# Kernel optimization log

Hardware: AMD Instinct MI355X
Metric: run time of the kernel (lower is better)

Reference implementation:

```python
import jax, jax.numpy as jnp
import numpy as np

N_PAPER = 50000
N_AUTHOR = 50000
E = 400000
N_FEAT = 256
N_HID = 256
N_CLASS = 128
TEMP = 1.0  # cfg.temparature


def setup_inputs() -> dict:
    key = jax.random.key(0)
    ks = jax.random.split(key, 40)
    def lin_init(k, shape, fan_in):
        s = 1.0 / np.sqrt(fan_in)
        return jax.random.uniform(k, shape, jnp.float32, -s, s)
    inp = {}
    inp['x_paper'] = jax.random.normal(ks[0], (N_PAPER, N_FEAT), jnp.float32)
    # xavier-uniform embedding for featureless node type 'author'
    xs = np.sqrt(6.0 / (N_AUTHOR + N_FEAT))
    inp['emb_author'] = jax.random.uniform(ks[1], (N_AUTHOR, N_FEAT), jnp.float32, -xs, xs)
    i = 2
    for l, fin in [(0, N_FEAT), (1, N_HID)]:
        for nt in ['paper', 'author']:
            inp[f'l{l}_root_{nt}_W'] = lin_init(ks[i], (fin, N_HID), fin); i += 1
            inp[f'l{l}_root_{nt}_b'] = lin_init(ks[i], (N_HID,), fin); i += 1
        for et in ['writes', 'rev', 'cites']:
            inp[f'l{l}_rel_{et}_W'] = lin_init(ks[i], (fin, N_HID), fin); i += 1
    inp['out_W'] = lin_init(ks[i], (N_HID, N_CLASS), N_HID); i += 1
    inp['out_b'] = lin_init(ks[i], (N_CLASS,), N_HID); i += 1
    inp['writes_src'] = jax.random.randint(ks[i], (E,), 0, N_AUTHOR); i += 1
    inp['writes_dst'] = jax.random.randint(ks[i], (E,), 0, N_PAPER); i += 1
    inp['rev_src'] = jax.random.randint(ks[i], (E,), 0, N_PAPER); i += 1
    inp['rev_dst'] = jax.random.randint(ks[i], (E,), 0, N_AUTHOR); i += 1
    inp['cites_src'] = jax.random.randint(ks[i], (E,), 0, N_PAPER); i += 1
    inp['cites_dst'] = jax.random.randint(ks[i], (E,), 0, N_PAPER); i += 1
    return inp


def _mean_agg(x_src, src, dst, n_dst):
    # sparse adj_t.matmul(x, reduce='mean'): segment-sum of gathered rows / in-degree (0 for isolated)
    msg = jax.ops.segment_sum(x_src[src], dst, num_segments=n_dst)  # [n_dst, d]
    deg = jax.ops.segment_sum(jnp.ones(src.shape[0], x_src.dtype), dst, num_segments=n_dst)
    return jnp.where(deg[:, None] > 0, msg / jnp.maximum(deg, 1.0)[:, None], 0.0)


def reference(x_paper, emb_author,
              l0_root_paper_W, l0_root_paper_b, l0_root_author_W, l0_root_author_b,
              l0_rel_writes_W, l0_rel_rev_W, l0_rel_cites_W,
              l1_root_paper_W, l1_root_paper_b, l1_root_author_W, l1_root_author_b,
              l1_rel_writes_W, l1_rel_rev_W, l1_rel_cites_W,
              out_W, out_b,
              writes_src, writes_dst, rev_src, rev_dst, cites_src, cites_dst):
    nnodes = {'paper': x_paper.shape[0], 'author': emb_author.shape[0]}
    # (src_type, dst_type, src_idx, dst_idx, rel_slot)
    edges = [('author', 'paper', writes_src, writes_dst, 0),
             ('paper', 'author', rev_src, rev_dst, 1),
             ('paper', 'paper', cites_src, cites_dst, 2)]
    layers = [
        {'root': {'paper': (l0_root_paper_W, l0_root_paper_b), 'author': (l0_root_author_W, l0_root_author_b)},
         'rel': [l0_rel_writes_W, l0_rel_rev_W, l0_rel_cites_W]},
        {'root': {'paper': (l1_root_paper_W, l1_root_paper_b), 'author': (l1_root_author_W, l1_root_author_b)},
         'rel': [l1_rel_writes_W, l1_rel_rev_W, l1_rel_cites_W]},
    ]
    xd = {'paper': x_paper, 'author': emb_author}
    xd_ = dict(xd)  # twin path starts from same features
    hs, hs_ = [], []
    for p in layers:
        out = {k: xd[k] @ p['root'][k][0] + p['root'][k][1] for k in xd}
        out_ = {k: xd_[k] @ p['root'][k][0] + p['root'][k][1] for k in xd_}
        for s, d, src, dst, slot in edges:
            W = p['rel'][slot]
            out[d] = out[d] + _mean_agg(xd[s], src, dst, nnodes[d]) @ W
            out_[d] = out_[d] + xd_[d] @ W  # twin path: no propagation, same rel transform
        xd = {k: jax.nn.relu(v) for k, v in out.items()}   # dropout is identity (eval)
        xd_ = {k: jax.nn.relu(v) for k, v in out_.items()}
        hs.append(xd['paper'])
        hs_.append(xd_['paper'])
    # Summarize: per-node dot-product attention over layer representations
    H = jnp.stack(hs)    # [L, N, d]
    H_ = jnp.stack(hs_)  # [L, N, d]
    alpha = jax.nn.softmax(jnp.sum(H * H_, axis=-1) / TEMP, axis=0)  # [L, N]
    h = jnp.sum(alpha[..., None] * H, axis=0)  # [N, d]
    logits = h @ out_W + out_b
    return (logits, alpha)
```

## Files before the change

kernel.cpp:

```cpp
#include <hip/hip_runtime.h>
#include <hip/hip_bf16.h>

#define NFEAT 256
#define BM 64
#define BN 64
#define BK 16

typedef __attribute__((ext_vector_type(8))) short bf16x8;
typedef __attribute__((ext_vector_type(4))) float f32x4;
typedef __attribute__((ext_vector_type(8))) unsigned short us8;

__device__ __forceinline__ void f2hilo(float x, unsigned short& h, unsigned short& l) {
    __hip_bfloat16 hb = __float2bfloat16(x);
    float hf = __bfloat162float(hb);
    __hip_bfloat16 lb = __float2bfloat16(x - hf);
    h = *reinterpret_cast<unsigned short*>(&hb);
    l = *reinterpret_cast<unsigned short*>(&lb);
}

__global__ __launch_bounds__(256) void addw3_kernel(const float* __restrict__ a,
                                                    const float* __restrict__ b,
                                                    const float* __restrict__ c,
                                                    float* __restrict__ o, int n) {
    int i = blockIdx.x * 256 + threadIdx.x;
    if (i < n) o[i] = a[i] + b[i] + c[i];
}

__global__ __launch_bounds__(256) void cvtW_kernel(const float* __restrict__ W, int K, int N,
                                                   unsigned short* __restrict__ Th,
                                                   unsigned short* __restrict__ Tl) {
    int idx = blockIdx.x * 256 + threadIdx.x;
    if (idx >= K * N) return;
    int k = idx / N, c = idx - k * N;
    unsigned short h, l;
    f2hilo(W[idx], h, l);
    Th[(size_t)c * K + k] = h;
    Tl[(size_t)c * K + k] = l;
}

__global__ __launch_bounds__(256) void deg_int_kernel(const int* __restrict__ dst,
                                                      int* __restrict__ deg, int nE) {
    int e = blockIdx.x * 256 + threadIdx.x;
    if (e < nE) atomicAdd(&deg[dst[e]], 1);
}

__global__ __launch_bounds__(256) void scan_p1(const int* __restrict__ deg, int n,
                                               int* __restrict__ off, int* __restrict__ bsum) {
    __shared__ int tmp[256];
    int tid = threadIdx.x;
    int i = blockIdx.x * 256 + tid;
    tmp[tid] = (i < n) ? deg[i] : 0;
    __syncthreads();
    #pragma unroll
    for (int ofs = 1; ofs < 256; ofs <<= 1) {
        int t = (tid >= ofs) ? tmp[tid - ofs] : 0;
        __syncthreads();
        tmp[tid] += t;
        __syncthreads();
    }
    if (i < n) off[i + 1] = tmp[tid];
    if (tid == 255) bsum[blockIdx.x] = tmp[255];
}

__global__ __launch_bounds__(256) void scan_p2(int* __restrict__ bA, int nA,
                                               int* __restrict__ bB, int nB,
                                               int* __restrict__ bC, int nC) {
    int* bs; int nb;
    if (blockIdx.x == 0) { bs = bA; nb = nA; }
    else if (blockIdx.x == 1) { bs = bB; nb = nB; }
    else { bs = bC; nb = nC; }
    __shared__ int tmp[256];
    int tid = threadIdx.x;
    tmp[tid] = (tid < nb) ? bs[tid] : 0;
    __syncthreads();
    #pragma unroll
    for (int ofs = 1; ofs < 256; ofs <<= 1) {
        int t = (tid >= ofs) ? tmp[tid - ofs] : 0;
        __syncthreads();
        tmp[tid] += t;
        __syncthreads();
    }
    if (tid < nb) bs[tid] = tmp[tid];
}

__global__ __launch_bounds__(256) void scan_p3(int n, int* __restrict__ off,
                                               const int* __restrict__ bsum) {
    int i = blockIdx.x * 256 + threadIdx.x;
    if (i == 0) off[0] = 0;
    if (i >= n) return;
    int b = blockIdx.x;
    if (b > 0) off[i + 1] += bsum[b - 1];
}

__global__ __launch_bounds__(256) void fill_csr_kernel(const int* __restrict__ src,
                                                       const int* __restrict__ dst, int nE,
                                                       const int* __restrict__ off,
                                                       int* __restrict__ cursor,
                                                       int* __restrict__ list) {
    int e = blockIdx.x * 256 + threadIdx.x;
    if (e >= nE) return;
    int d = dst[e];
    int pos = atomicAdd(&cursor[d], 1);
    list[off[d] + pos] = src[e];
}

__global__ __launch_bounds__(256) void agg_csr_kernel(const float* __restrict__ T,
                                                      const int* __restrict__ off,
                                                      const int* __restrict__ list,
                                                      float* __restrict__ D,
                                                      int do_relu, int M) {
    int r = blockIdx.x * 4 + (threadIdx.x >> 6);
    if (r >= M) return;
    int lane = threadIdx.x & 63;
    int start = off[r], end = off[r + 1];
    float4 acc = make_float4(0.f, 0.f, 0.f, 0.f);
    for (int e = start; e < end; ++e) {
        int s = list[e];
        float4 v = ((const float4*)(T + (size_t)s * NFEAT))[lane];
        acc.x += v.x; acc.y += v.y; acc.z += v.z; acc.w += v.w;
    }
    int cnt = end - start;
    float inv = (cnt > 0) ? 1.0f / (float)cnt : 0.0f;
    float4 d = ((float4*)(D + (size_t)r * NFEAT))[lane];
    d.x += acc.x * inv; d.y += acc.y * inv;
    d.z += acc.z * inv; d.w += acc.w * inv;
    if (do_relu) {
        d.x = fmaxf(d.x, 0.f); d.y = fmaxf(d.y, 0.f);
        d.z = fmaxf(d.z, 0.f); d.w = fmaxf(d.w, 0.f);
    }
    ((float4*)(D + (size_t)r * NFEAT))[lane] = d;
}

__global__ __launch_bounds__(256) void rowdot_kernel(const float* __restrict__ A,
                                                     const float* __restrict__ B,
                                                     float* __restrict__ s, int M) {
    int n = blockIdx.x * 4 + (threadIdx.x >> 6);
    if (n >= M) return;
    int lane = threadIdx.x & 63;
    float4 a = ((const float4*)(A + (size_t)n * NFEAT))[lane];
    float4 b = ((const float4*)(B + (size_t)n * NFEAT))[lane];
    float d = a.x * b.x + a.y * b.y + a.z * b.z + a.w * b.w;
    #pragma unroll
    for (int off = 32; off > 0; off >>= 1) d += __shfl_down(d, off);
    if (lane == 0) s[n] = d;
}

__global__ __launch_bounds__(256) void combine_kernel(const float* __restrict__ P1,
                                                      const float* __restrict__ P2,
                                                      const float* __restrict__ s0,
                                                      const float* __restrict__ s1,
                                                      float* __restrict__ h,
                                                      float* __restrict__ alpha,
                                                      int M) {
    int n = blockIdx.x * 4 + (threadIdx.x >> 6);
    if (n >= M) return;
    int lane = threadIdx.x & 63;
    float v0 = s0[n], v1 = s1[n];
    float m = fmaxf(v0, v1);
    float e0 = expf(v0 - m), e1 = expf(v1 - m);
    float inv = 1.0f / (e0 + e1);
    float a0 = e0 * inv, a1 = e1 * inv;
    float4 p1 = ((const float4*)(P1 + (size_t)n * NFEAT))[lane];
    float4 p2 = ((const float4*)(P2 + (size_t)n * NFEAT))[lane];
    float4 hv;
    hv.x = a0 * p1.x + a1 * p2.x;
    hv.y = a0 * p1.y + a1 * p2.y;
    hv.z = a0 * p1.z + a1 * p2.z;
    hv.w = a0 * p1.w + a1 * p2.w;
    ((float4*)(h + (size_t)n * NFEAT))[lane] = hv;
    if (lane == 0) {
        alpha[n]     = a0;
        alpha[M + n] = a1;
    }
}

__global__ __launch_bounds__(256, 2) void gemm_mfma(
    const float* __restrict__ X,
    const unsigned short* __restrict__ Wh,
    const unsigned short* __restrict__ Wl,
    const float* __restrict__ bias, int do_relu,
    float* __restrict__ C, int M, int N)
{
    __shared__ unsigned short Ah[128][40];
    __shared__ unsigned short Al[128][40];
    __shared__ unsigned short Bh[128][40];
    __shared__ unsigned short Bl[128][40];

    int tid = threadIdx.x;
    int lane = tid & 63;
    int w = tid >> 6;
    int wr = w >> 1, wc = w & 1;
    int row0 = blockIdx.x * 128, col0 = blockIdx.y * 128;

    int sr = tid >> 1;
    int sk = (tid & 1) * 16;

    int grow = row0 + sr; if (grow >= M) grow = M - 1;
    const float* Xrow = X + (size_t)grow * NFEAT;
    const unsigned short* Whrow = Wh + (size_t)(col0 + sr) * NFEAT;
    const unsigned short* Wlrow = Wl + (size_t)(col0 + sr) * NFEAT;

    f32x4 acc[4][4];
    #pragma unroll
    for (int m = 0; m < 4; ++m)
        #pragma unroll
        for (int n = 0; n < 4; ++n)
            acc[m][n] = (f32x4)(0.f);

    int fr = lane & 15;
    int fg = lane >> 4;

    for (int k0 = 0; k0 < NFEAT; k0 += 32) {
        unsigned short hh[16], ll[16];
        #pragma unroll
        for (int q = 0; q < 4; ++q) {
            float4 v = *(const float4*)(Xrow + k0 + sk + q * 4);
            f2hilo(v.x, hh[q*4+0], ll[q*4+0]);
            f2hilo(v.y, hh[q*4+1], ll[q*4+1]);
            f2hilo(v.z, hh[q*4+2], ll[q*4+2]);
            f2hilo(v.w, hh[q*4+3], ll[q*4+3]);
        }
        us8 bh0 = *(const us8*)(Whrow + k0 + sk);
        us8 bh1 = *(const us8*)(Whrow + k0 + sk + 8);
        us8 bl0 = *(const us8*)(Wlrow + k0 + sk);
        us8 bl1 = *(const us8*)(Wlrow + k0 + sk + 8);
        __syncthreads();
        *(us8*)&Ah[sr][sk]     = *(us8*)&hh[0];
        *(us8*)&Ah[sr][sk + 8] = *(us8*)&hh[8];
        *(us8*)&Al[sr][sk]     = *(us8*)&ll[0];
        *(us8*)&Al[sr][sk + 8] = *(us8*)&ll[8];
        *(us8*)&Bh[sr][sk]     = bh0;
        *(us8*)&Bh[sr][sk + 8] = bh1;
        *(us8*)&Bl[sr][sk]     = bl0;
        *(us8*)&Bl[sr][sk + 8] = bl1;
        __syncthreads();

        bf16x8 ah[4], al[4], bhf[4], blf[4];
        #pragma unroll
        for (int m = 0; m < 4; ++m) {
            int r = wr * 64 + m * 16 + fr;
            ah[m] = *(const bf16x8*)&Ah[r][fg * 8];
            al[m] = *(const bf16x8*)&Al[r][fg * 8];
        }
        #pragma unroll
        for (int n = 0; n < 4; ++n) {
            int c = wc * 64 + n * 16 + fr;
            bhf[n] = *(const bf16x8*)&Bh[c][fg * 8];
            blf[n] = *(const bf16x8*)&Bl[c][fg * 8];
        }
        #pragma unroll
        for (int m = 0; m < 4; ++m)
            #pragma unroll
            for (int n = 0; n < 4; ++n) {
                acc[m][n] = __builtin_amdgcn_mfma_f32_16x16x32_bf16(ah[m], bhf[n], acc[m][n], 0, 0, 0);
                acc[m][n] = __builtin_amdgcn_mfma_f32_16x16x32_bf16(al[m], bhf[n], acc[m][n], 0, 0, 0);
                acc[m][n] = __builtin_amdgcn_mfma_f32_16x16x32_bf16(ah[m], blf[n], acc[m][n], 0, 0, 0);
            }
    }

    #pragma unroll
    for (int n = 0; n < 4; ++n) {
        int c = col0 + wc * 64 + n * 16 + fr;
        float bv = bias ? bias[c] : 0.f;
        #pragma unroll
        for (int m = 0; m < 4; ++m) {
            int rbase = row0 + wr * 64 + m * 16 + fg * 4;
            #pragma unroll
            for (int i = 0; i < 4; ++i) {
                int r = rbase + i;
                if (r < M) {
                    float v = acc[m][n][i] + bv;
                    if (do_relu) v = fmaxf(v, 0.f);
                    C[(size_t)r * N + c] = v;
                }
            }
        }
    }
}

__global__ __launch_bounds__(256) void gemm_rowdot_kernel(
    const float* __restrict__ X, const float* __restrict__ W,
    const float* __restrict__ bias, const float* __restrict__ P,
    float* __restrict__ s, int M)
{
    __shared__ float Xs[BK][BM];
    __shared__ float Ws[BK][BN];
    __shared__ float srow[BM];

    int tid = threadIdx.x;
    int row0 = blockIdx.x * BM;

    int lr = tid & 63;
    int lk = (tid >> 6) * 4;
    int wk = tid >> 4;
    int wc = (tid & 15) * 4;
    int ty = tid >> 4;
    int tx = tid & 15;

    int grow = row0 + lr;
    if (grow >= M) grow = M - 1;

    if (tid < BM) srow[tid] = 0.f;

    float rp[4] = {0.f, 0.f, 0.f, 0.f};

    for (int col0 = 0; col0 < NFEAT; col0 += BN) {
        float acc[4][4] = {{0.f}};
        for (int k0 = 0; k0 < NFEAT; k0 += BK) {
            float4 xv = *(const float4*)(X + (size_t)grow * NFEAT + k0 + lk);
            float4 wv = *(const float4*)(W + (size_t)(k0 + wk) * NFEAT + col0 + wc);
            __syncthreads();
            Xs[lk + 0][lr] = xv.x;
            Xs[lk + 1][lr] = xv.y;
            Xs[lk + 2][lr] = xv.z;
            Xs[lk + 3][lr] = xv.w;
            *(float4*)&Ws[wk][wc] = wv;
            __syncthreads();
            #pragma unroll
            for (int kk = 0; kk < BK; ++kk) {
                float4 a = *(const float4*)&Xs[kk][ty * 4];
                float4 b = *(const float4*)&Ws[kk][tx * 4];
                acc[0][0] += a.x * b.x; acc[0][1] += a.x * b.y;
                acc[0][2] += a.x * b.z; acc[0][3] += a.x * b.w;
                acc[1][0] += a.y * b.x; acc[1][1] += a.y * b.y;
                acc[1][2] += a.y * b.z; acc[1][3] += a.y * b.w;
                acc[2][0] += a.z * b.x; acc[2][1] += a.z * b.y;
                acc[2][2] += a.z * b.z; acc[2][3] += a.z * b.w;
                acc[3][0] += a.w * b.x; acc[3][1] += a.w * b.y;
                acc[3][2] += a.w * b.z; acc[3][3] += a.w * b.w;
            }
        }
        int c0 = col0 + tx * 4;
        #pragma unroll
        for (int i = 0; i < 4; ++i) {
            int r = row0 + ty * 4 + i;
            if (r >= M) continue;
            float4 p = *(const float4*)(P + (size_t)r * NFEAT + c0);
            float v0 = fmaxf(acc[i][0] + bias[c0 + 0], 0.f);
            float v1 = fmaxf(acc[i][1] + bias[c0 + 1], 0.f);
            float v2 = fmaxf(acc[i][2] + bias[c0 + 2], 0.f);
            float v3 = fmaxf(acc[i][3] + bias[c0 + 3], 0.f);
            rp[i] += v0 * p.x + v1 * p.y + v2 * p.z + v3 * p.w;
        }
    }
    __syncthreads();
    #pragma unroll
    for (int i = 0; i < 4; ++i) atomicAdd(&srow[ty * 4 + i], rp[i]);
    __syncthreads();
    if (tid < BM && row0 + tid < M) s[row0 + tid] = srow[tid];
}

extern "C" void kernel_launch(void* const* d_in, const int* in_sizes, int n_in,
                              void* d_out, int out_size, void* d_ws, size_t ws_size,
                              hipStream_t stream)
{
    const float* x_paper    = (const float*)d_in[0];
    const float* emb_author = (const float*)d_in[1];
    const float* W0rp = (const float*)d_in[2];
    const float* b0rp = (const float*)d_in[3];
    const float* W0ra = (const float*)d_in[4];
    const float* b0ra = (const float*)d_in[5];
    const float* W0w  = (const float*)d_in[6];
    const float* W0rev= (const float*)d_in[7];
    const float* W0c  = (const float*)d_in[8];
    const float* W1rp = (const float*)d_in[9];
    const float* b1rp = (const float*)d_in[10];
    const float* W1w  = (const float*)d_in[13];
    const float* W1c  = (const float*)d_in[15];
    const float* outW = (const float*)d_in[16];
    const float* outb = (const float*)d_in[17];
    const int* w_src = (const int*)d_in[18];
    const int* w_dst = (const int*)d_in[19];
    const int* r_src = (const int*)d_in[20];
    const int* r_dst = (const int*)d_in[21];
    const int* c_src = (const int*)d_in[22];
    const int* c_dst = (const int*)d_in[23];

    const int NP = in_sizes[0] / NFEAT;
    const int NA = in_sizes[1] / NFEAT;
    const int NC = in_sizes[17];
    const int nEw = in_sizes[18], nEr = in_sizes[20], nEc = in_sizes[22];

    size_t NB = (size_t)(NP > NA ? NP : NA) * NFEAT;
    float* Z1 = (float*)d_ws;
    float* Z2 = Z1 + NB;
    float* Z3 = Z2 + NB;
    float* s0   = Z3 + NB;
    float* s1   = s0 + NP;
    float* Wc0f = s1 + NP;
    float* Wc1f = Wc0f + NFEAT * NFEAT;
    unsigned short* Wt = (unsigned short*)(Wc1f + NFEAT * NFEAT);
    const size_t WSLOT = 2 * 65536;
    #define WT_HI(i) (Wt + (size_t)(i) * WSLOT)
    #define WT_LO(i) (Wt + (size_t)(i) * WSLOT + 65536)
    int* ib   = (int*)(Wt + 11 * WSLOT);
    int* degW = ib;
    int* degR = degW + NP;
    int* degC = degR + NA;
    int* curW = degC + NP;
    int* curR = curW + NP;
    int* curC = curR + NA;
    int* offW = curC + NP;
    int* offR = offW + NP + 1;
    int* offC = offR + NA + 1;
    int* bsW  = offC + NP + 1;
    int* bsR  = bsW + 256;
    int* bsC  = bsR + 256;
    int* listW = bsC + 256;
    int* listR = listW + nEw;
    int* listC = listR + nEr;

    float* out   = (float*)d_out;
    float* alpha = out + (size_t)NP * NC;

    hipMemsetAsync(degW, 0, (size_t)2 * (NP + NA + NP) * sizeof(int), stream);

    deg_int_kernel<<<(nEw + 255) / 256, 256, 0, stream>>>(w_dst, degW, nEw);
    deg_int_kernel<<<(nEr + 255) / 256, 256, 0, stream>>>(r_dst, degR, nEr);
    deg_int_kernel<<<(nEc + 255) / 256, 256, 0, stream>>>(c_dst, degC, nEc);

    int nbP = (NP + 255) / 256, nbA = (NA + 255) / 256;
    scan_p1<<<nbP, 256, 0, stream>>>(degW, NP, offW, bsW);
    scan_p1<<<nbA, 256, 0, stream>>>(degR, NA, offR, bsR);
    scan_p1<<<nbP, 256, 0, stream>>>(degC, NP, offC, bsC);
    scan_p2<<<3, 256, 0, stream>>>(bsW, nbP, bsR, nbA, bsC, nbP);
    scan_p3<<<nbP, 256, 0, stream>>>(NP, offW, bsW);
    scan_p3<<<nbA, 256, 0, stream>>>(NA, offR, bsR);
    scan_p3<<<nbP, 256, 0, stream>>>(NP, offC, bsC);

    fill_csr_kernel<<<(nEw + 255) / 256, 256, 0, stream>>>(w_src, w_dst, nEw, offW, curW, listW);
    fill_csr_kernel<<<(nEr + 255) / 256, 256, 0, stream>>>(r_src, r_dst, nEr, offR, curR, listR);
    fill_csr_kernel<<<(nEc + 255) / 256, 256, 0, stream>>>(c_src, c_dst, nEc, offC, curC, listC);

    int nW = NFEAT * NFEAT;
    int wblk = (nW + 255) / 256;
    addw3_kernel<<<wblk, 256, 0, stream>>>(W0rp, W0w, W0c, Wc0f, nW);
    addw3_kernel<<<wblk, 256, 0, stream>>>(W1rp, W1w, W1c, Wc1f, nW);

    cvtW_kernel<<<wblk, 256, 0, stream>>>(W0rp, NFEAT, NFEAT, WT_HI(0), WT_LO(0));
    cvtW_kernel<<<wblk, 256, 0, stream>>>(W0w,  NFEAT, NFEAT, WT_HI(1), WT_LO(1));
    cvtW_kernel<<<wblk, 256, 0, stream>>>(W0c,  NFEAT, NFEAT, WT_HI(2), WT_LO(2));
    cvtW_kernel<<<wblk, 256, 0, stream>>>(W0ra, NFEAT, NFEAT, WT_HI(3), WT_LO(3));
    cvtW_kernel<<<wblk, 256, 0, stream>>>(W0rev,NFEAT, NFEAT, WT_HI(4), WT_LO(4));
    cvtW_kernel<<<wblk, 256, 0, stream>>>(W1w,  NFEAT, NFEAT, WT_HI(5), WT_LO(5));
    cvtW_kernel<<<wblk, 256, 0, stream>>>(W1rp, NFEAT, NFEAT, WT_HI(6), WT_LO(6));
    cvtW_kernel<<<wblk, 256, 0, stream>>>(W1c,  NFEAT, NFEAT, WT_HI(7), WT_LO(7));
    cvtW_kernel<<<wblk, 256, 0, stream>>>(Wc0f, NFEAT, NFEAT, WT_HI(8), WT_LO(8));
    cvtW_kernel<<<(NFEAT * NC + 255) / 256, 256, 0, stream>>>(outW, NFEAT, NC, WT_HI(9), WT_LO(9));

    dim3 blk(256);
    dim3 gM((NP + 127) / 128, NFEAT / 128);
    dim3 gMA((NA + 127) / 128, NFEAT / 128);
    dim3 gMO((NP + 127) / 128, NC / 128);
    dim3 gR((NP + BM - 1) / BM);
    int nodeP = (NP + 3) / 4, nodeA = (NA + 3) / 4;

    gemm_mfma<<<gM, blk, 0, stream>>>(x_paper, WT_HI(0), WT_LO(0), b0rp, 0, Z1, NP, NFEAT);
    gemm_mfma<<<gMA, blk, 0, stream>>>(emb_author, WT_HI(1), WT_LO(1), nullptr, 0, Z2, NA, NFEAT);
    agg_csr_kernel<<<nodeP, blk, 0, stream>>>(Z2, offW, listW, Z1, 0, NP);
    gemm_mfma<<<gM, blk, 0, stream>>>(x_paper, WT_HI(2), WT_LO(2), nullptr, 0, Z2, NP, NFEAT);
    agg_csr_kernel<<<nodeP, blk, 0, stream>>>(Z2, offC, listC, Z1, 1, NP);

    gemm_mfma<<<gMA, blk, 0, stream>>>(emb_author, WT_HI(3), WT_LO(3), b0ra, 0, Z2, NA, NFEAT);
    gemm_mfma<<<gM, blk, 0, stream>>>(x_paper, WT_HI(4), WT_LO(4), nullptr, 0, Z3, NP, NFEAT);
    agg_csr_kernel<<<nodeA, blk, 0, stream>>>(Z3, offR, listR, Z2, 1, NA);

    gemm_mfma<<<gMA, blk, 0, stream>>>(Z2, WT_HI(5), WT_LO(5), nullptr, 0, Z3, NA, NFEAT);
    gemm_mfma<<<gM, blk, 0, stream>>>(Z1, WT_HI(6), WT_LO(6), b1rp, 0, Z2, NP, NFEAT);
    agg_csr_kernel<<<nodeP, blk, 0, stream>>>(Z3, offW, listW, Z2, 0, NP);
    gemm_mfma<<<gM, blk, 0, stream>>>(Z1, WT_HI(7), WT_LO(7), nullptr, 0, Z3, NP, NFEAT);
    agg_csr_kernel<<<nodeP, blk, 0, stream>>>(Z3, offC, listC, Z2, 1, NP);

    gemm_mfma<<<gM, blk, 0, stream>>>(x_paper, WT_HI(8), WT_LO(8), b0rp, 1, Z3, NP, NFEAT);
    rowdot_kernel<<<nodeP, blk, 0, stream>>>(Z1, Z3, s0, NP);
    gemm_rowdot_kernel<<<gR, blk, 0, stream>>>(Z3, Wc1f, b1rp, Z2, s1, NP);

    combine_kernel<<<nodeP, blk, 0, stream>>>(Z1, Z2, s0, s1, Z3, alpha, NP);
    gemm_mfma<<<gMO, blk, 0, stream>>>(Z3, WT_HI(9), WT_LO(9), outb, 0, out, NP, NC);
}
```

Measured before the change: 1.090 ms.

## Aggregate raw features first and fuse multi-segment GEMMs, rowdot and head

Reorders each relation to aggregate input features before the transform ((A·X)·W instead of A·(X·W)). A new multi-segment GEMM then sums the root and relation products in one kernel with bias and ReLU, which removes separate read-modify-write aggregation passes and several GEMM launches. The twin-path score, rowdot and final combine are fused into MFMA-based GEMM kernels, and weight conversion is batched into fewer launches. This trades extra live accumulator segments per block for fewer full-size intermediate round trips through memory.

```diff
diff --git a/kernel.cpp b/kernel.cpp
--- a/kernel.cpp
+++ b/kernel.cpp
@@ -2,13 +2,14 @@
 #include <hip/hip_bf16.h>
 
 #define NFEAT 256
-#define BM 64
-#define BN 64
-#define BK 16
 
 typedef __attribute__((ext_vector_type(8))) short bf16x8;
 typedef __attribute__((ext_vector_type(4))) float f32x4;
 typedef __attribute__((ext_vector_type(8))) unsigned short us8;
+
+__device__ __forceinline__ float bf2f(unsigned short u) {
+    union { unsigned int i; float f; } v; v.i = ((unsigned int)u) << 16; return v.f;
+}
 
 __device__ __forceinline__ void f2hilo(float x, unsigned short& h, unsigned short& l) {
     __hip_bfloat16 hb = __float2bfloat16(x);
@@ -18,24 +19,48 @@
     l = *reinterpret_cast<unsigned short*>(&lb);
 }
 
-__global__ __launch_bounds__(256) void addw3_kernel(const float* __restrict__ a,
-                                                    const float* __restrict__ b,
-                                                    const float* __restrict__ c,
-                                                    float* __restrict__ o, int n) {
-    int i = blockIdx.x * 256 + threadIdx.x;
-    if (i < n) o[i] = a[i] + b[i] + c[i];
-}
-
-__global__ __launch_bounds__(256) void cvtW_kernel(const float* __restrict__ W, int K, int N,
-                                                   unsigned short* __restrict__ Th,
-                                                   unsigned short* __restrict__ Tl) {
+__global__ __launch_bounds__(256) void cvt8_kernel(
+    const float* w0, const float* w1, const float* w2, const float* w3,
+    const float* w4, const float* w5, const float* w6, const float* w7,
+    unsigned short* base)
+{
+    int wi = blockIdx.y;
+    const float* W = (wi==0)?w0:(wi==1)?w1:(wi==2)?w2:(wi==3)?w3:
+                     (wi==4)?w4:(wi==5)?w5:(wi==6)?w6:w7;
     int idx = blockIdx.x * 256 + threadIdx.x;
-    if (idx >= K * N) return;
-    int k = idx / N, c = idx - k * N;
+    int k = idx >> 8, c = idx & 255;
     unsigned short h, l;
     f2hilo(W[idx], h, l);
-    Th[(size_t)c * K + k] = h;
-    Tl[(size_t)c * K + k] = l;
+    unsigned short* Th = base + (size_t)wi * 131072;
+    Th[c * 256 + k] = h;
+    Th[65536 + c * 256 + k] = l;
+}
+
+__global__ __launch_bounds__(256) void cvtfold_kernel(
+    const float* a0, const float* a1, const float* a2,
+    const float* b0, const float* b1, const float* b2,
+    unsigned short* base)
+{
+    int wi = blockIdx.y;
+    int idx = blockIdx.x * 256 + threadIdx.x;
+    float v = wi ? (b0[idx] + b1[idx] + b2[idx]) : (a0[idx] + a1[idx] + a2[idx]);
+    int k = idx >> 8, c = idx & 255;
+    unsigned short h, l;
+    f2hilo(v, h, l);
+    unsigned short* Th = base + (size_t)(8 + wi) * 131072;
+    Th[c * 256 + k] = h;
+    Th[65536 + c * 256 + k] = l;
+}
+
+__global__ __launch_bounds__(256) void cvtrect_kernel(const float* W, unsigned short* base) {
+    int idx = blockIdx.x * 256 + threadIdx.x;
+    if (idx >= 256 * 128) return;
+    int k = idx >> 7, c = idx & 127;
+    unsigned short h, l;
+    f2hilo(W[idx], h, l);
+    unsigned short* Th = base + (size_t)10 * 131072;
+    Th[c * 256 + k] = h;
+    Th[65536 + c * 256 + k] = l;
 }
 
 __global__ __launch_bounds__(256) void deg_int_kernel(const int* __restrict__ dst,
@@ -108,7 +133,7 @@
                                                       const int* __restrict__ off,
                                                       const int* __restrict__ list,
                                                       float* __restrict__ D,
-                                                      int do_relu, int M) {
+                                                      int mode_add, int do_relu, int M) {
     int r = blockIdx.x * 4 + (threadIdx.x >> 6);
     if (r >= M) return;
     int lane = threadIdx.x & 63;
@@ -121,9 +146,15 @@
     }
     int cnt = end - start;
     float inv = (cnt > 0) ? 1.0f / (float)cnt : 0.0f;
-    float4 d = ((float4*)(D + (size_t)r * NFEAT))[lane];
-    d.x += acc.x * inv; d.y += acc.y * inv;
-    d.z += acc.z * inv; d.w += acc.w * inv;
+    float4 d;
+    if (mode_add) {
+        d = ((float4*)(D + (size_t)r * NFEAT))[lane];
+        d.x += acc.x * inv; d.y += acc.y * inv;
+        d.z += acc.z * inv; d.w += acc.w * inv;
+    } else {
+        d.x = acc.x * inv; d.y = acc.y * inv;
+        d.z = acc.z * inv; d.w = acc.w * inv;
+    }
     if (do_relu) {
         d.x = fmaxf(d.x, 0.f); d.y = fmaxf(d.y, 0.f);
         d.z = fmaxf(d.z, 0.f); d.w = fmaxf(d.w, 0.f);
@@ -131,54 +162,26 @@
     ((float4*)(D + (size_t)r * NFEAT))[lane] = d;
 }
 
-__global__ __launch_bounds__(256) void rowdot_kernel(const float* __restrict__ A,
-                                                     const float* __restrict__ B,
-                                                     float* __restrict__ s, int M) {
-    int n = blockIdx.x * 4 + (threadIdx.x >> 6);
+__global__ __launch_bounds__(256) void alpha_kernel(const float* __restrict__ s0,
+                                                    const float* __restrict__ s1,
+                                                    float* __restrict__ alpha, int M) {
+    int n = blockIdx.x * 256 + threadIdx.x;
     if (n >= M) return;
-    int lane = threadIdx.x & 63;
-    float4 a = ((const float4*)(A + (size_t)n * NFEAT))[lane];
-    float4 b = ((const float4*)(B + (size_t)n * NFEAT))[lane];
-    float d = a.x * b.x + a.y * b.y + a.z * b.z + a.w * b.w;
-    #pragma unroll
-    for (int off = 32; off > 0; off >>= 1) d += __shfl_down(d, off);
-    if (lane == 0) s[n] = d;
-}
-
-__global__ __launch_bounds__(256) void combine_kernel(const float* __restrict__ P1,
-                                                      const float* __restrict__ P2,
-                                                      const float* __restrict__ s0,
-                                                      const float* __restrict__ s1,
-                                                      float* __restrict__ h,
-                                                      float* __restrict__ alpha,
-                                                      int M) {
-    int n = blockIdx.x * 4 + (threadIdx.x >> 6);
-    if (n >= M) return;
-    int lane = threadIdx.x & 63;
     float v0 = s0[n], v1 = s1[n];
     float m = fmaxf(v0, v1);
     float e0 = expf(v0 - m), e1 = expf(v1 - m);
     float inv = 1.0f / (e0 + e1);
-    float a0 = e0 * inv, a1 = e1 * inv;
-    float4 p1 = ((const float4*)(P1 + (size_t)n * NFEAT))[lane];
-    float4 p2 = ((const float4*)(P2 + (size_t)n * NFEAT))[lane];
-    float4 hv;
-    hv.x = a0 * p1.x + a1 * p2.x;
-    hv.y = a0 * p1.y + a1 * p2.y;
-    hv.z = a0 * p1.z + a1 * p2.z;
-    hv.w = a0 * p1.w + a1 * p2.w;
-    ((float4*)(h + (size_t)n * NFEAT))[lane] = hv;
-    if (lane == 0) {
-        alpha[n]     = a0;
-        alpha[M + n] = a1;
-    }
-}
-
-__global__ __launch_bounds__(256, 2) void gemm_mfma(
-    const float* __restrict__ X,
-    const unsigned short* __restrict__ Wh,
-    const unsigned short* __restrict__ Wl,
-    const float* __restrict__ bias, int do_relu,
+    alpha[n]     = e0 * inv;
+    alpha[M + n] = e1 * inv;
+}
+
+struct Seg3 {
+    const float *A0, *A1, *A2;
+    const unsigned short *Wh0, *Wl0, *Wh1, *Wl1, *Wh2, *Wl2;
+};
+
+__global__ __launch_bounds__(256, 2) void gemm_ms(
+    Seg3 sp, int nseg, const float* __restrict__ bias, int do_relu,
     float* __restrict__ C, int M, int N)
 {
     __shared__ unsigned short Ah[128][40];
@@ -191,14 +194,11 @@
     int w = tid >> 6;
     int wr = w >> 1, wc = w & 1;
     int row0 = blockIdx.x * 128, col0 = blockIdx.y * 128;
-
     int sr = tid >> 1;
     int sk = (tid & 1) * 16;
-
     int grow = row0 + sr; if (grow >= M) grow = M - 1;
-    const float* Xrow = X + (size_t)grow * NFEAT;
-    const unsigned short* Whrow = Wh + (size_t)(col0 + sr) * NFEAT;
-    const unsigned short* Wlrow = Wl + (size_t)(col0 + sr) * NFEAT;
+    int fr = lane & 15;
+    int fg = lane >> 4;
 
     f32x4 acc[4][4];
     #pragma unroll
@@ -207,14 +207,264 @@
         for (int n = 0; n < 4; ++n)
             acc[m][n] = (f32x4)(0.f);
 
+    for (int s = 0; s < 3; ++s) {
+        if (s >= nseg) break;
+        const float* Xrow = ((s == 0) ? sp.A0 : (s == 1) ? sp.A1 : sp.A2) + (size_t)grow * NFEAT;
+        const unsigned short* Whrow = ((s == 0) ? sp.Wh0 : (s == 1) ? sp.Wh1 : sp.Wh2) + (size_t)(col0 + sr) * NFEAT;
+        const unsigned short* Wlrow = ((s == 0) ? sp.Wl0 : (s == 1) ? sp.Wl1 : sp.Wl2) + (size_t)(col0 + sr) * NFEAT;
+
+        for (int k0 = 0; k0 < NFEAT; k0 += 32) {
+            unsigned short hh[16], ll[16];
+            #pragma unroll
+            for (int q = 0; q < 4; ++q) {
+                float4 v = *(const float4*)(Xrow + k0 + sk + q * 4);
+                f2hilo(v.x, hh[q*4+0], ll[q*4+0]);
+                f2hilo(v.y, hh[q*4+1], ll[q*4+1]);
+                f2hilo(v.z, hh[q*4+2], ll[q*4+2]);
+                f2hilo(v.w, hh[q*4+3], ll[q*4+3]);
+            }
+            us8 bh0 = *(const us8*)(Whrow + k0 + sk);
+            us8 bh1 = *(const us8*)(Whrow + k0 + sk + 8);
+            us8 bl0 = *(const us8*)(Wlrow + k0 + sk);
+            us8 bl1 = *(const us8*)(Wlrow + k0 + sk + 8);
+            __syncthreads();
+            *(us8*)&Ah[sr][sk]     = *(us8*)&hh[0];
+            *(us8*)&Ah[sr][sk + 8] = *(us8*)&hh[8];
+            *(us8*)&Al[sr][sk]     = *(us8*)&ll[0];
+            *(us8*)&Al[sr][sk + 8] = *(us8*)&ll[8];
+            *(us8*)&Bh[sr][sk]     = bh0;
+            *(us8*)&Bh[sr][sk + 8] = bh1;
+            *(us8*)&Bl[sr][sk]     = bl0;
+            *(us8*)&Bl[sr][sk + 8] = bl1;
+            __syncthreads();
+
+            bf16x8 ah[4], al[4], bhf[4], blf[4];
+            #pragma unroll
+            for (int m = 0; m < 4; ++m) {
+                int r = wr * 64 + m * 16 + fr;
+                ah[m] = *(const bf16x8*)&Ah[r][fg * 8];
+                al[m] = *(const bf16x8*)&Al[r][fg * 8];
+            }
+            #pragma unroll
+            for (int n = 0; n < 4; ++n) {
+                int c = wc * 64 + n * 16 + fr;
+                bhf[n] = *(const bf16x8*)&Bh[c][fg * 8];
+                blf[n] = *(const bf16x8*)&Bl[c][fg * 8];
+            }
+            #pragma unroll
+            for (int m = 0; m < 4; ++m)
+                #pragma unroll
+                for (int n = 0; n < 4; ++n) {
+                    acc[m][n] = __builtin_amdgcn_mfma_f32_16x16x32_bf16(ah[m], bhf[n], acc[m][n], 0, 0, 0);
+                    acc[m][n] = __builtin_amdgcn_mfma_f32_16x16x32_bf16(al[m], bhf[n], acc[m][n], 0, 0, 0);
+                    acc[m][n] = __builtin_amdgcn_mfma_f32_16x16x32_bf16(ah[m], blf[n], acc[m][n], 0, 0, 0);
+                }
+        }
+    }
+
+    #pragma unroll
+    for (int n = 0; n < 4; ++n) {
+        int c = col0 + wc * 64 + n * 16 + fr;
+        float bv = bias ? bias[c] : 0.f;
+        #pragma unroll
+        for (int m = 0; m < 4; ++m) {
+            int rbase = row0 + wr * 64 + m * 16 + fg * 4;
+            #pragma unroll
+            for (int i = 0; i < 4; ++i) {
+                int r = rbase + i;
+                if (r < M) {
+                    float v = acc[m][n][i] + bv;
+                    if (do_relu) v = fmaxf(v, 0.f);
+                    C[(size_t)r * N + c] = v;
+                }
+            }
+        }
+    }
+}
+
+__global__ __launch_bounds__(256, 2) void gemm_rowdot_mfma(
+    const float* __restrict__ X,
+    const unsigned short* __restrict__ Wh, const unsigned short* __restrict__ Wl,
+    const float* __restrict__ bias,
+    const float* __restrict__ P, const float* __restrict__ Q,
+    float* __restrict__ s0g, float* __restrict__ s1g, int M)
+{
+    __shared__ unsigned short Ah[128][40];
+    __shared__ unsigned short Al[128][40];
+    __shared__ unsigned short Bh[128][40];
+    __shared__ unsigned short Bl[128][40];
+    __shared__ float srow[128];
+
+    int tid = threadIdx.x;
+    int lane = tid & 63;
+    int w = tid >> 6;
+    int wr = w >> 1, wc = w & 1;
+    int row0 = blockIdx.x * 128;
+    int sr = tid >> 1;
+    int sk = (tid & 1) * 16;
+    int grow = row0 + sr; if (grow >= M) grow = M - 1;
     int fr = lane & 15;
     int fg = lane >> 4;
 
+    const float* Xrow = X + (size_t)grow * NFEAT;
+    const float* Qrow = Q + (size_t)grow * NFEAT;
+
+    if (tid < 128) srow[tid] = 0.f;
+    float s0part = 0.f;
+    float rp[4][4];
+    #pragma unroll
+    for (int m = 0; m < 4; ++m)
+        #pragma unroll
+        for (int i = 0; i < 4; ++i) rp[m][i] = 0.f;
+
+    for (int ct = 0; ct < 2; ++ct) {
+        int col0 = ct * 128;
+        const unsigned short* Whrow = Wh + (size_t)(col0 + sr) * NFEAT;
+        const unsigned short* Wlrow = Wl + (size_t)(col0 + sr) * NFEAT;
+
+        f32x4 acc[4][4];
+        #pragma unroll
+        for (int m = 0; m < 4; ++m)
+            #pragma unroll
+            for (int n = 0; n < 4; ++n)
+                acc[m][n] = (f32x4)(0.f);
+
+        for (int k0 = 0; k0 < NFEAT; k0 += 32) {
+            unsigned short hh[16], ll[16];
+            #pragma unroll
+            for (int q = 0; q < 4; ++q) {
+                float4 v = *(const float4*)(Xrow + k0 + sk + q * 4);
+                if (ct == 0) {
+                    float4 qv = *(const float4*)(Qrow + k0 + sk + q * 4);
+                    s0part += v.x * qv.x + v.y * qv.y + v.z * qv.z + v.w * qv.w;
+                }
+                f2hilo(v.x, hh[q*4+0], ll[q*4+0]);
+                f2hilo(v.y, hh[q*4+1], ll[q*4+1]);
+                f2hilo(v.z, hh[q*4+2], ll[q*4+2]);
+                f2hilo(v.w, hh[q*4+3], ll[q*4+3]);
+            }
+            us8 bh0 = *(const us8*)(Whrow + k0 + sk);
+            us8 bh1 = *(const us8*)(Whrow + k0 + sk + 8);
+            us8 bl0 = *(const us8*)(Wlrow + k0 + sk);
+            us8 bl1 = *(const us8*)(Wlrow + k0 + sk + 8);
+            __syncthreads();
+            *(us8*)&Ah[sr][sk]     = *(us8*)&hh[0];
+            *(us8*)&Ah[sr][sk + 8] = *(us8*)&hh[8];
+            *(us8*)&Al[sr][sk]     = *(us8*)&ll[0];
+            *(us8*)&Al[sr][sk + 8] = *(us8*)&ll[8];
+            *(us8*)&Bh[sr][sk]     = bh0;
+            *(us8*)&Bh[sr][sk + 8] = bh1;
+            *(us8*)&Bl[sr][sk]     = bl0;
+            *(us8*)&Bl[sr][sk + 8] = bl1;
+            __syncthreads();
+
+            bf16x8 ah[4], al[4], bhf[4], blf[4];
+            #pragma unroll
+            for (int m = 0; m < 4; ++m) {
+                int r = wr * 64 + m * 16 + fr;
+                ah[m] = *(const bf16x8*)&Ah[r][fg * 8];
+                al[m] = *(const bf16x8*)&Al[r][fg * 8];
+            }
+            #pragma unroll
+            for (int n = 0; n < 4; ++n) {
+                int c = wc * 64 + n * 16 + fr;
+                bhf[n] = *(const bf16x8*)&Bh[c][fg * 8];
+                blf[n] = *(const bf16x8*)&Bl[c][fg * 8];
+            }
+            #pragma unroll
+            for (int m = 0; m < 4; ++m)
+                #pragma unroll
+                for (int n = 0; n < 4; ++n) {
+                    acc[m][n] = __builtin_amdgcn_mfma_f32_16x16x32_bf16(ah[m], bhf[n], acc[m][n], 0, 0, 0);
+                    acc[m][n] = __builtin_amdgcn_mfma_f32_16x16x32_bf16(al[m], bhf[n], acc[m][n], 0, 0, 0);
+                    acc[m][n] = __builtin_amdgcn_mfma_f32_16x16x32_bf16(ah[m], blf[n], acc[m][n], 0, 0, 0);
+                }
+        }
+
+        #pragma unroll
+        for (int n = 0; n < 4; ++n) {
+            int c = col0 + wc * 64 + n * 16 + fr;
+            float bv = bias[c];
+            #pragma unroll
+            for (int m = 0; m < 4; ++m) {
+                #pragma unroll
+                for (int i = 0; i < 4; ++i) {
+                    int r = row0 + wr * 64 + m * 16 + fg * 4 + i;
+                    if (r < M) {
+                        float v = fmaxf(acc[m][n][i] + bv, 0.f);
+                        rp[m][i] += v * P[(size_t)r * NFEAT + c];
+                    }
+                }
+            }
+        }
+    }
+
+    #pragma unroll
+    for (int o = 1; o < 16; o <<= 1) {
+        #pragma unroll
+        for (int m = 0; m < 4; ++m)
+            #pragma unroll
+            for (int i = 0; i < 4; ++i)
+                rp[m][i] += __shfl_xor(rp[m][i], o);
+    }
+    if ((lane & 15) == 0) {
+        #pragma unroll
+        for (int m = 0; m < 4; ++m)
+            #pragma unroll
+            for (int i = 0; i < 4; ++i)
+                atomicAdd(&srow[wr * 64 + m * 16 + fg * 4 + i], rp[m][i]);
+    }
+    s0part += __shfl_xor(s0part, 1);
+    if ((tid & 1) == 0 && row0 + sr < M) s0g[row0 + sr] = s0part;
+    __syncthreads();
+    if (tid < 128 && row0 + tid < M) s1g[row0 + tid] = srow[tid];
+}
+
+__global__ __launch_bounds__(256, 2) void gemm_head(
+    const float* __restrict__ P1, const float* __restrict__ P2,
+    const float* __restrict__ alpha,
+    const unsigned short* __restrict__ Wh, const unsigned short* __restrict__ Wl,
+    const float* __restrict__ bias,
+    float* __restrict__ C, int M, int N)
+{
+    __shared__ unsigned short Ah[128][40];
+    __shared__ unsigned short Al[128][40];
+    __shared__ unsigned short Bh[128][40];
+    __shared__ unsigned short Bl[128][40];
+
+    int tid = threadIdx.x;
+    int lane = tid & 63;
+    int w = tid >> 6;
+    int wr = w >> 1, wc = w & 1;
+    int row0 = blockIdx.x * 128;
+    int sr = tid >> 1;
+    int sk = (tid & 1) * 16;
+    int grow = row0 + sr; if (grow >= M) grow = M - 1;
+    int fr = lane & 15;
+    int fg = lane >> 4;
+
+    const float* P1row = P1 + (size_t)grow * NFEAT;
+    const float* P2row = P2 + (size_t)grow * NFEAT;
+    float a0 = alpha[grow], a1 = alpha[M + grow];
+
+    f32x4 acc[4][4];
+    #pragma unroll
+    for (int m = 0; m < 4; ++m)
+        #pragma unroll
+        for (int n = 0; n < 4; ++n)
+            acc[m][n] = (f32x4)(0.f);
+
+    const unsigned short* Whrow = Wh + (size_t)sr * NFEAT;
+    const unsigned short* Wlrow = Wl + (size_t)sr * NFEAT;
+
     for (int k0 = 0; k0 < NFEAT; k0 += 32) {
         unsigned short hh[16], ll[16];
         #pragma unroll
         for (int q = 0; q < 4; ++q) {
-            float4 v = *(const float4*)(Xrow + k0 + sk + q * 4);
+            float4 v1 = *(const float4*)(P1row + k0 + sk + q * 4);
+            float4 v2 = *(const float4*)(P2row + k0 + sk + q * 4);
+            float4 v = make_float4(a0 * v1.x + a1 * v2.x, a0 * v1.y + a1 * v2.y,
+                                   a0 * v1.z + a1 * v2.z, a0 * v1.w + a1 * v2.w);
             f2hilo(v.x, hh[q*4+0], ll[q*4+0]);
             f2hilo(v.y, hh[q*4+1], ll[q*4+1]);
             f2hilo(v.z, hh[q*4+2], ll[q*4+2]);
@@ -260,94 +510,19 @@
 
     #pragma unroll
     for (int n = 0; n < 4; ++n) {
-        int c = col0 + wc * 64 + n * 16 + fr;
-        float bv = bias ? bias[c] : 0.f;
+        int c = wc * 64 + n * 16 + fr;
+        if (c >= N) continue;
+        float bv = bias[c];
         #pragma unroll
         for (int m = 0; m < 4; ++m) {
             int rbase = row0 + wr * 64 + m * 16 + fg * 4;
             #pragma unroll
             for (int i = 0; i < 4; ++i) {
                 int r = rbase + i;
-                if (r < M) {
-                    float v = acc[m][n][i] + bv;
-                    if (do_relu) v = fmaxf(v, 0.f);
-                    C[(size_t)r * N + c] = v;
-                }
-            }
-        }
-    }
-}
-
-__global__ __launch_bounds__(256) void gemm_rowdot_kernel(
-    const float* __restrict__ X, const float* __restrict__ W,
-    const float* __restrict__ bias, const float* __restrict__ P,
-    float* __restrict__ s, int M)
-{
-    __shared__ float Xs[BK][BM];
-    __shared__ float Ws[BK][BN];
-    __shared__ float srow[BM];
-
-    int tid = threadIdx.x;
-    int row0 = blockIdx.x * BM;
-
-    int lr = tid & 63;
-    int lk = (tid >> 6) * 4;
-    int wk = tid >> 4;
-    int wc = (tid & 15) * 4;
-    int ty = tid >> 4;
-    int tx = tid & 15;
-
-    int grow = row0 + lr;
-    if (grow >= M) grow = M - 1;
-
-    if (tid < BM) srow[tid] = 0.f;
-
-    float rp[4] = {0.f, 0.f, 0.f, 0.f};
-
-    for (int col0 = 0; col0 < NFEAT; col0 += BN) {
-        float acc[4][4] = {{0.f}};
-        for (int k0 = 0; k0 < NFEAT; k0 += BK) {
-            float4 xv = *(const float4*)(X + (size_t)grow * NFEAT + k0 + lk);
-            float4 wv = *(const float4*)(W + (size_t)(k0 + wk) * NFEAT + col0 + wc);
-            __syncthreads();
-            Xs[lk + 0][lr] = xv.x;
-            Xs[lk + 1][lr] = xv.y;
-            Xs[lk + 2][lr] = xv.z;
-            Xs[lk + 3][lr] = xv.w;
-            *(float4*)&Ws[wk][wc] = wv;
-            __syncthreads();
-            #pragma unroll
-            for (int kk = 0; kk < BK; ++kk) {
-                float4 a = *(const float4*)&Xs[kk][ty * 4];
-                float4 b = *(const float4*)&Ws[kk][tx * 4];
-                acc[0][0] += a.x * b.x; acc[0][1] += a.x * b.y;
-                acc[0][2] += a.x * b.z; acc[0][3] += a.x * b.w;
-                acc[1][0] += a.y * b.x; acc[1][1] += a.y * b.y;
-                acc[1][2] += a.y * b.z; acc[1][3] += a.y * b.w;
-                acc[2][0] += a.z * b.x; acc[2][1] += a.z * b.y;
-                acc[2][2] += a.z * b.z; acc[2][3] += a.z * b.w;
-                acc[3][0] += a.w * b.x; acc[3][1] += a.w * b.y;
-                acc[3][2] += a.w * b.z; acc[3][3] += a.w * b.w;
-            }
-        }
-        int c0 = col0 + tx * 4;
-        #pragma unroll
-        for (int i = 0; i < 4; ++i) {
-            int r = row0 + ty * 4 + i;
-            if (r >= M) continue;
-            float4 p = *(const float4*)(P + (size_t)r * NFEAT + c0);
-            float v0 = fmaxf(acc[i][0] + bias[c0 + 0], 0.f);
-            float v1 = fmaxf(acc[i][1] + bias[c0 + 1], 0.f);
-            float v2 = fmaxf(acc[i][2] + bias[c0 + 2], 0.f);
-            float v3 = fmaxf(acc[i][3] + bias[c0 + 3], 0.f);
-            rp[i] += v0 * p.x + v1 * p.y + v2 * p.z + v3 * p.w;
-        }
-    }
-    __syncthreads();
-    #pragma unroll
-    for (int i = 0; i < 4; ++i) atomicAdd(&srow[ty * 4 + i], rp[i]);
-    __syncthreads();
-    if (tid < BM && row0 + tid < M) s[row0 + tid] = srow[tid];
+                if (r < M) C[(size_t)r * N + c] = acc[m][n][i] + bv;
+            }
+        }
+    }
 }
 
 extern "C" void kernel_launch(void* const* d_in, const int* in_sizes, int n_in,
@@ -382,19 +557,15 @@
     const int nEw = in_sizes[18], nEr = in_sizes[20], nEc = in_sizes[22];
 
     size_t NB = (size_t)(NP > NA ? NP : NA) * NFEAT;
-    float* Z1 = (float*)d_ws;
+    float* Z0 = (float*)d_ws;
+    float* Z1 = Z0 + NB;
     float* Z2 = Z1 + NB;
-    float* Z3 = Z2 + NB;
-    float* s0   = Z3 + NB;
-    float* s1   = s0 + NP;
-    float* Wc0f = s1 + NP;
-    float* Wc1f = Wc0f + NFEAT * NFEAT;
-    unsigned short* Wt = (unsigned short*)(Wc1f + NFEAT * NFEAT);
-    const size_t WSLOT = 2 * 65536;
-    #define WT_HI(i) (Wt + (size_t)(i) * WSLOT)
-    #define WT_LO(i) (Wt + (size_t)(i) * WSLOT + 65536)
-    int* ib   = (int*)(Wt + 11 * WSLOT);
-    int* degW = ib;
+    float* s0 = Z2 + NB;
+    float* s1 = s0 + NP;
+    unsigned short* Wt = (unsigned short*)(s1 + NP);
+    #define WT_HI(i) (Wt + (size_t)(i) * 131072)
+    #define WT_LO(i) (Wt + (size_t)(i) * 131072 + 65536)
+    int* degW = (int*)(Wt + 11 * 131072);
     int* degR = degW + NP;
     int* degC = degR + NA;
     int* curW = degC + NP;
@@ -414,7 +585,6 @@
     float* alpha = out + (size_t)NP * NC;
 
     hipMemsetAsync(degW, 0, (size_t)2 * (NP + NA + NP) * sizeof(int), stream);
-
     deg_int_kernel<<<(nEw + 255) / 256, 256, 0, stream>>>(w_dst, degW, nEw);
     deg_int_kernel<<<(nEr + 255) / 256, 256, 0, stream>>>(r_dst, degR, nEr);
     deg_int_kernel<<<(nEc + 255) / 256, 256, 0, stream>>>(c_dst, degC, nEc);
@@ -432,49 +602,45 @@
     fill_csr_kernel<<<(nEr + 255) / 256, 256, 0, stream>>>(r_src, r_dst, nEr, offR, curR, listR);
     fill_csr_kernel<<<(nEc + 255) / 256, 256, 0, stream>>>(c_src, c_dst, nEc, offC, curC, listC);
 
-    int nW = NFEAT * NFEAT;
-    int wblk = (nW + 255) / 256;
-    addw3_kernel<<<wblk, 256, 0, stream>>>(W0rp, W0w, W0c, Wc0f, nW);
-    addw3_kernel<<<wblk, 256, 0, stream>>>(W1rp, W1w, W1c, Wc1f, nW);
-
-    cvtW_kernel<<<wblk, 256, 0, stream>>>(W0rp, NFEAT, NFEAT, WT_HI(0), WT_LO(0));
-    cvtW_kernel<<<wblk, 256, 0, stream>>>(W0w,  NFEAT, NFEAT, WT_HI(1), WT_LO(1));
-    cvtW_kernel<<<wblk, 256, 0, stream>>>(W0c,  NFEAT, NFEAT, WT_HI(2), WT_LO(2));
-    cvtW_kernel<<<wblk, 256, 0, stream>>>(W0ra, NFEAT, NFEAT, WT_HI(3), WT_LO(3));
-    cvtW_kernel<<<wblk, 256, 0, stream>>>(W0rev,NFEAT, NFEAT, WT_HI(4), WT_LO(4));
-    cvtW_kernel<<<wblk, 256, 0, stream>>>(W1w,  NFEAT, NFEAT, WT_HI(5), WT_LO(5));
-    cvtW_kernel<<<wblk, 256, 0, stream>>>(W1rp, NFEAT, NFEAT, WT_HI(6), WT_LO(6));
-    cvtW_kernel<<<wblk, 256, 0, stream>>>(W1c,  NFEAT, NFEAT, WT_HI(7), WT_LO(7));
-    cvtW_kernel<<<wblk, 256, 0, stream>>>(Wc0f, NFEAT, NFEAT, WT_HI(8), WT_LO(8));
-    cvtW_kernel<<<(NFEAT * NC + 255) / 256, 256, 0, stream>>>(outW, NFEAT, NC, WT_HI(9), WT_LO(9));
+    cvt8_kernel<<<dim3(256, 8), 256, 0, stream>>>(W0rp, W0w, W0c, W0ra, W0rev, W1rp, W1w, W1c, Wt);
+    cvtfold_kernel<<<dim3(256, 2), 256, 0, stream>>>(W0rp, W0w, W0c, W1rp, W1w, W1c, Wt);
+    cvtrect_kernel<<<128, 256, 0, stream>>>(outW, Wt);
 
     dim3 blk(256);
-    dim3 gM((NP + 127) / 128, NFEAT / 128);
-    dim3 gMA((NA + 127) / 128, NFEAT / 128);
-    dim3 gMO((NP + 127) / 128, NC / 128);
-    dim3 gR((NP + BM - 1) / BM);
+    dim3 gP((NP + 127) / 128, 2);
+    dim3 gA((NA + 127) / 128, 2);
+    dim3 g1((NP + 127) / 128);
     int nodeP = (NP + 3) / 4, nodeA = (NA + 3) / 4;
 
-    gemm_mfma<<<gM, blk, 0, stream>>>(x_paper, WT_HI(0), WT_LO(0), b0rp, 0, Z1, NP, NFEAT);
-    gemm_mfma<<<gMA, blk, 0, stream>>>(emb_author, WT_HI(1), WT_LO(1), nullptr, 0, Z2, NA, NFEAT);
-    agg_csr_kernel<<<nodeP, blk, 0, stream>>>(Z2, offW, listW, Z1, 0, NP);
-    gemm_mfma<<<gM, blk, 0, stream>>>(x_paper, WT_HI(2), WT_LO(2), nullptr, 0, Z2, NP, NFEAT);
-    agg_csr_kernel<<<nodeP, blk, 0, stream>>>(Z2, offC, listC, Z1, 1, NP);
-
-    gemm_mfma<<<gMA, blk, 0, stream>>>(emb_author, WT_HI(3), WT_LO(3), b0ra, 0, Z2, NA, NFEAT);
-    gemm_mfma<<<gM, blk, 0, stream>>>(x_paper, WT_HI(4), WT_LO(4), nullptr, 0, Z3, NP, NFEAT);
-    agg_csr_kernel<<<nodeA, blk, 0, stream>>>(Z3, offR, listR, Z2, 1, NA);
-
-    gemm_mfma<<<gMA, blk, 0, stream>>>(Z2, WT_HI(5), WT_LO(5), nullptr, 0, Z3, NA, NFEAT);
-    gemm_mfma<<<gM, blk, 0, stream>>>(Z1, WT_HI(6), WT_LO(6), b1rp, 0, Z2, NP, NFEAT);
-    agg_csr_kernel<<<nodeP, blk, 0, stream>>>(Z3, offW, listW, Z2, 0, NP);
-    gemm_mfma<<<gM, blk, 0, stream>>>(Z1, WT_HI(7), WT_LO(7), nullptr, 0, Z3, NP, NFEAT);
-    agg_csr_kernel<<<nodeP, blk, 0, stream>>>(Z3, offC, listC, Z2, 1, NP);
-
-    gemm_mfma<<<gM, blk, 0, stream>>>(x_paper, WT_HI(8), WT_LO(8), b0rp, 1, Z3, NP, NFEAT);
-    rowdot_kernel<<<nodeP, blk, 0, stream>>>(Z1, Z3, s0, NP);
-    gemm_rowdot_kernel<<<gR, blk, 0, stream>>>(Z3, Wc1f, b1rp, Z2, s1, NP);
-
-    combine_kernel<<<nodeP, blk, 0, stream>>>(Z1, Z2, s0, s1, Z3, alpha, NP);
-    gemm_mfma<<<gMO, blk, 0, stream>>>(Z3, WT_HI(9), WT_LO(9), outb, 0, out, NP, NC);
-}
+    agg_csr_kernel<<<nodeP, blk, 0, stream>>>(emb_author, offW, listW, Z0, 0, 0, NP);
+    agg_csr_kernel<<<nodeP, blk, 0, stream>>>(x_paper,    offC, listC, Z1, 0, 0, NP);
+    {
+        Seg3 sp = {x_paper, Z0, Z1, WT_HI(0), WT_LO(0), WT_HI(1), WT_LO(1), WT_HI(2), WT_LO(2)};
+        gemm_ms<<<gP, blk, 0, stream>>>(sp, 3, b0rp, 1, Z2, NP, NFEAT);
+    }
+    agg_csr_kernel<<<nodeA, blk, 0, stream>>>(x_paper, offR, listR, Z0, 0, 0, NA);
+    {
+        Seg3 sp = {emb_author, Z0, nullptr, WT_HI(3), WT_LO(3), WT_HI(4), WT_LO(4), nullptr, nullptr};
+        gemm_ms<<<gA, blk, 0, stream>>>(sp, 2, b0ra, 1, Z1, NA, NFEAT);
+    }
+
+    agg_csr_kernel<<<nodeP, blk, 0, stream>>>(Z1, offW, listW, Z0, 0, 0, NP);
+    {
+        Seg3 sp = {Z2, Z0, nullptr, WT_HI(5), WT_LO(5), WT_HI(6), WT_LO(6), nullptr, nullptr};
+        gemm_ms<<<gP, blk, 0, stream>>>(sp, 2, b1rp, 0, Z1, NP, NFEAT);
+    }
+    {
+        Seg3 sp = {Z2, nullptr, nullptr, WT_HI(7), WT_LO(7), nullptr, nullptr, nullptr, nullptr};
+        gemm_ms<<<gP, blk, 0, stream>>>(sp, 1, nullptr, 0, Z0, NP, NFEAT);
+    }
+    agg_csr_kernel<<<nodeP, blk, 0, stream>>>(Z0, offC, listC, Z1, 1, 1, NP);
+
+    {
+        Seg3 sp = {x_paper, nullptr, nullptr, WT_HI(8), WT_LO(8), nullptr, nullptr, nullptr, nullptr};
+        gemm_ms<<<gP, blk, 0, stream>>>(sp, 1, b0rp, 1, Z0, NP, NFEAT);
+    }
+    gemm_rowdot_mfma<<<g1, blk, 0, stream>>>(Z0, WT_HI(9), WT_LO(9), b1rp, Z1, Z2, s0, s1, NP);
+
+    alpha_kernel<<<(NP + 255) / 256, blk, 0, stream>>>(s0, s1, alpha, NP);
+    gemm_head<<<g1, blk, 0, stream>>>(Z2, Z1, alpha, WT_HI(10), WT_LO(10), outb, out, NP, NC);
+}
```

After: 879.3 us. 19.3% less time.
